# Optimization experiments

Measured on AMD Instinct MI355X. Metric: run time of the kernel, lower is better.

The kernel has to match this reference:

```python
import jax, jax.numpy as jnp
import numpy as np

HIDDEN = 128
POOL = 64
G = 4            # grid_size
NBHD = 2.0       # neighborhood_size (meters)
NUM_SCENES = 256
PEDS = 64        # pedestrians per scene (uniform seq_start_end)


def setup_inputs() -> dict:
    key = jax.random.key(0)
    k1, k2, k3 = jax.random.split(key, 3)
    hidden_states = jax.random.normal(k1, (NUM_SCENES * PEDS, HIDDEN), jnp.float32)
    positions = jax.random.uniform(k2, (NUM_SCENES * PEDS, 2), jnp.float32)
    fan_in = HIDDEN * G * G
    weight = jax.random.normal(k3, (fan_in, POOL), jnp.float32) / np.sqrt(fan_in)
    bias = jnp.zeros((POOL,), jnp.float32)
    return {
        "hidden_states": hidden_states,
        "positions": positions,
        "weight": weight,
        "bias": bias,
        "peds_per_scene": PEDS,
    }


def reference(hidden_states, positions, weight, bias, peds_per_scene):
    total, H = hidden_states.shape
    P = peds_per_scene
    B = total // P
    h = hidden_states.reshape(B, P, H)
    p = positions.reshape(B, P, 2)

    # rel[b, i, j] = pos[j] - pos[i]  (matches curr_pos - curr_pos[i:i+1])
    rel = p[:, None, :, :] - p[:, :, None, :]            # [B, P, P, 2]
    in_range = (jnp.abs(rel[..., 0]) <= NBHD) & (jnp.abs(rel[..., 1]) <= NBHD)
    not_self = ~jnp.eye(P, dtype=bool)[None]
    mask = in_range & not_self                            # [B, P, P]

    # int() truncation == floor here since (rel + NBHD) >= 0 inside the range check
    scale = G / (2.0 * NBHD)
    gx = jnp.clip(jnp.floor((rel[..., 0] + NBHD) * scale).astype(jnp.int32), 0, G - 1)
    gy = jnp.clip(jnp.floor((rel[..., 1] + NBHD) * scale).astype(jnp.int32), 0, G - 1)
    grid_idx = gy * G + gx                                # [B, P, P]

    # scatter-add of neighbor hidden states into G*G bins via masked one-hot
    onehot = jax.nn.one_hot(grid_idx, G * G, dtype=h.dtype) * mask[..., None].astype(h.dtype)
    grid = jnp.einsum('bijg,bjh->bigh', onehot, h)        # [B, P, G*G, H]

    flat = grid.reshape(B * P, G * G * H)                 # row-major: (grid_idx, hidden)
    return flat @ weight + bias                            # [total_peds, POOL]
```

## Files before the change

kernel.cpp:

```cpp
#include <hip/hip_runtime.h>
#include <cstdint>

#define PEDS   64
#define HIDDEN 128
#define POOL   64
#define GRIDG  4
#define NBHD   2.0f

typedef unsigned short u16;
typedef unsigned int   u32;
typedef __attribute__((ext_vector_type(8))) short bf16x8;
typedef __attribute__((ext_vector_type(4))) float f32x4;

__device__ __forceinline__ u16 f2bf(float f) {
    u32 u = __float_as_uint(f);
    u += 0x7fffu + ((u >> 16) & 1u);
    return (u16)(u >> 16);
}
__device__ __forceinline__ u32 pack2bf(float a, float b) {
    return (u32)f2bf(a) | ((u32)f2bf(b) << 16);
}

__global__ __launch_bounds__(256, 3) void social_r6(
    const float* __restrict__ h, const float* __restrict__ pos,
    const float* __restrict__ w, const float* __restrict__ bias,
    float* __restrict__ out)
{
    __shared__ u16 wtab[16384];
    __shared__ u16 hwT[8192];
    __shared__ u32 wmask[4];

    const int tid  = threadIdx.x;
    const int wv   = tid >> 6;
    const int lane = tid & 63;
    const int l15  = lane & 15;
    const int q    = lane >> 4;
    const int scene = blockIdx.x >> 1;
    const int ch    = blockIdx.x & 1;

    float2 pp = ((const float2*)pos)[(size_t)scene * PEDS + lane];

    const int i = wv * 16 + l15;
    const float pxi = __shfl(pp.x, i), pyi = __shfl(pp.y, i);
    const float scale = (float)GRIDG / (2.0f * NBHD);
    u32 gpk[4] = {0u, 0u, 0u, 0u};
    u32 um = 0u;
#pragma unroll
    for (int kk = 0; kk < 2; ++kk) {
#pragma unroll
        for (int e = 0; e < 8; ++e) {
            int j = kk * 32 + q * 8 + e;
            float rx = __shfl(pp.x, j) - pxi;
            float ry = __shfl(pp.y, j) - pyi;
            u32 gb = 0xffu;
            if ((i != j) && (fabsf(rx) <= NBHD) && (fabsf(ry) <= NBHD)) {
                int gx = (int)floorf((rx + NBHD) * scale); gx = min(max(gx, 0), GRIDG - 1);
                int gy = (int)floorf((ry + NBHD) * scale); gy = min(max(gy, 0), GRIDG - 1);
                gb = (u32)(gy * GRIDG + gx);
                um |= 1u << gb;
            }
            gpk[kk * 2 + (e >> 2)] |= gb << ((e & 3) * 8);
        }
    }
#pragma unroll
    for (int off = 32; off; off >>= 1) um |= __shfl_xor(um, off);
    if (lane == 0) wmask[wv] = um;

    bf16x8 af[4];
    {
        const float* hr = h + ((size_t)scene * PEDS + wv * 16 + l15) * HIDDEN + q * 8;
#pragma unroll
        for (int st4 = 0; st4 < 4; ++st4) {
            float4 f0 = *(const float4*)(hr + st4 * 32);
            float4 f1 = *(const float4*)(hr + st4 * 32 + 4);
            union { u32 u[4]; bf16x8 v; } uu;
            uu.u[0] = pack2bf(f0.x, f0.y);
            uu.u[1] = pack2bf(f0.z, f0.w);
            uu.u[2] = pack2bf(f1.x, f1.y);
            uu.u[3] = pack2bf(f1.z, f1.w);
            af[st4] = uu.v;
        }
    }
    const float bv0 = bias[ch * 32 + l15];
    const float bv1 = bias[ch * 32 + 16 + l15];

    __syncthreads();
    u32 mask = wmask[0] | wmask[1] | wmask[2] | wmask[3];
    mask = __builtin_amdgcn_readfirstlane(mask);

    f32x4 oacc0 = (f32x4){0.f, 0.f, 0.f, 0.f};
    f32x4 oacc1 = (f32x4){0.f, 0.f, 0.f, 0.f};

    const int np = __popc(mask);
    const int nb = np ? (np + 3) >> 2 : 1;
    u32 rem = mask;

    const int tl    = tid & 127;
    const int c4    = tl & 7;
    const int koct  = tl >> 3;
    const int slot0 = (tid >> 7) * 2;

    for (int b = 0; b < nb; ++b) {
        int gs[4];
#pragma unroll
        for (int t = 0; t < 4; ++t) {
            gs[t] = rem ? (__ffs(rem) - 1) : -1;
            if (rem) rem &= rem - 1u;
        }
        if (b) __syncthreads();

#pragma unroll
        for (int tt = 0; tt < 2; ++tt) {
            int t  = slot0 + tt;
            int ge = gs[t] < 0 ? 0 : gs[t];
            const float* src = w + ((size_t)(ge * HIDDEN + koct * 8)) * POOL + ch * 32 + c4 * 4;
            float4 v[8];
#pragma unroll
            for (int e = 0; e < 8; ++e) v[e] = *(const float4*)(src + (size_t)e * POOL);
            const float* vp = (const float*)v;
            int st4 = koct >> 2, ni = c4 >> 2;
            int Lb  = (koct & 3) * 16 + (c4 & 3) * 4;
            uint4* dst = (uint4*)wtab + ((t * 4 + st4) * 2 + ni) * 64 + Lb;
#pragma unroll
            for (int ii = 0; ii < 4; ++ii) {
                dst[ii] = make_uint4(
                    pack2bf(vp[0 * 4 + ii], vp[1 * 4 + ii]),
                    pack2bf(vp[2 * 4 + ii], vp[3 * 4 + ii]),
                    pack2bf(vp[4 * 4 + ii], vp[5 * 4 + ii]),
                    pack2bf(vp[6 * 4 + ii], vp[7 * 4 + ii]));
            }
        }
        __syncthreads();

        const int kkw = wv >> 1;
        const int c4w = (wv & 1) * 2 + (q >> 1);
        const int e0  = (q & 1) * 4;
#pragma unroll
        for (int t = 0; t < 4; ++t) {
            f32x4 a10 = (f32x4){0.f, 0.f, 0.f, 0.f};
            f32x4 a11 = (f32x4){0.f, 0.f, 0.f, 0.f};
#pragma unroll
            for (int st4 = 0; st4 < 4; ++st4) {
                bf16x8 b0 = *(const bf16x8*)&wtab[(((t * 4 + st4) * 2 + 0) * 64 + lane) * 8];
                bf16x8 b1 = *(const bf16x8*)&wtab[(((t * 4 + st4) * 2 + 1) * 64 + lane) * 8];
                a10 = __builtin_amdgcn_mfma_f32_16x16x32_bf16(af[st4], b0, a10, 0, 0, 0);
                a11 = __builtin_amdgcn_mfma_f32_16x16x32_bf16(af[st4], b1, a11, 0, 0, 0);
            }
            *(uint2*)&hwT[((((t * 2 + kkw) * 4 + c4w) * 2 + 0) * 16 + l15) * 8 + e0] =
                make_uint2(pack2bf(a10[0], a10[1]), pack2bf(a10[2], a10[3]));
            *(uint2*)&hwT[((((t * 2 + kkw) * 4 + c4w) * 2 + 1) * 16 + l15) * 8 + e0] =
                make_uint2(pack2bf(a11[0], a11[1]), pack2bf(a11[2], a11[3]));
        }
        __syncthreads();

#pragma unroll
        for (int t = 0; t < 4; ++t) {
            u32 gt = (u32)gs[t];
#pragma unroll
            for (int kk = 0; kk < 2; ++kk) {
                u32 wa = gpk[kk * 2], wc = gpk[kk * 2 + 1];
                union { u16 hx[8]; bf16x8 v; } mu;
#pragma unroll
                for (int bb_ = 0; bb_ < 4; ++bb_)
                    mu.hx[bb_]     = (((wa >> (bb_ * 8)) & 0xffu) == gt) ? (u16)0x3F80 : (u16)0;
#pragma unroll
                for (int bb_ = 0; bb_ < 4; ++bb_)
                    mu.hx[4 + bb_] = (((wc >> (bb_ * 8)) & 0xffu) == gt) ? (u16)0x3F80 : (u16)0;
                bf16x8 bb0 = *(const bf16x8*)&hwT[((((t * 2 + kk) * 4 + q) * 2 + 0) * 16 + l15) * 8];
                bf16x8 bb1 = *(const bf16x8*)&hwT[((((t * 2 + kk) * 4 + q) * 2 + 1) * 16 + l15) * 8];
                oacc0 = __builtin_amdgcn_mfma_f32_16x16x32_bf16(mu.v, bb0, oacc0, 0, 0, 0);
                oacc1 = __builtin_amdgcn_mfma_f32_16x16x32_bf16(mu.v, bb1, oacc1, 0, 0, 0);
            }
        }
    }

    size_t ob = ((size_t)scene * PEDS + wv * 16 + q * 4) * POOL + ch * 32 + l15;
#pragma unroll
    for (int r = 0; r < 4; ++r) {
        out[ob + (size_t)r * POOL]      = oacc0[r] + bv0;
        out[ob + (size_t)r * POOL + 16] = oacc1[r] + bv1;
    }
}

extern "C" void kernel_launch(void* const* d_in, const int* in_sizes, int n_in,
                              void* d_out, int out_size, void* d_ws, size_t ws_size,
                              hipStream_t stream) {
    const float* h    = (const float*)d_in[0];
    const float* pos  = (const float*)d_in[1];
    const float* w    = (const float*)d_in[2];
    const float* bias = (const float*)d_in[3];
    float* out = (float*)d_out;

    const int total = in_sizes[0] / HIDDEN;
    const int B     = total / PEDS;

    hipLaunchKernelGGL(social_r6, dim3(B * 2), dim3(256), 0, stream,
                       h, pos, w, bias, out);
}
```

Measured before the change: 72.71 us.

## Prefetch weights for central grid bins before computing the occupancy mask

```diff
diff --git a/kernel.cpp b/kernel.cpp
--- a/kernel.cpp
+++ b/kernel.cpp
@@ -21,7 +21,7 @@
     return (u32)f2bf(a) | ((u32)f2bf(b) << 16);
 }
 
-__global__ __launch_bounds__(256, 3) void social_r6(
+__global__ __launch_bounds__(256, 2) void social_r7(
     const float* __restrict__ h, const float* __restrict__ pos,
     const float* __restrict__ w, const float* __restrict__ bias,
     float* __restrict__ out)
@@ -38,7 +38,47 @@
     const int scene = blockIdx.x >> 1;
     const int ch    = blockIdx.x & 1;
 
+    const u32 SPECMASK = (1u << 5) | (1u << 6) | (1u << 9) | (1u << 10);
+
     float2 pp = ((const float2*)pos)[(size_t)scene * PEDS + lane];
+    const float* hr = h + ((size_t)scene * PEDS + wv * 16 + l15) * HIDDEN + q * 8;
+    float4 hf[8];
+#pragma unroll
+    for (int st4 = 0; st4 < 4; ++st4) {
+        hf[st4 * 2]     = *(const float4*)(hr + st4 * 32);
+        hf[st4 * 2 + 1] = *(const float4*)(hr + st4 * 32 + 4);
+    }
+    const float bv0 = bias[ch * 32 + l15];
+    const float bv1 = bias[ch * 32 + 16 + l15];
+
+    const int tl    = tid & 127;
+    const int c4    = tl & 7;
+    const int koct  = tl >> 3;
+    const int slot0 = (tid >> 7) * 2;
+    {
+        const int spec[4] = {5, 6, 9, 10};
+#pragma unroll
+        for (int tt = 0; tt < 2; ++tt) {
+            int t  = slot0 + tt;
+            int ge = spec[t];
+            const float* src = w + ((size_t)(ge * HIDDEN + koct * 8)) * POOL + ch * 32 + c4 * 4;
+            float4 v[8];
+#pragma unroll
+            for (int e = 0; e < 8; ++e) v[e] = *(const float4*)(src + (size_t)e * POOL);
+            const float* vp = (const float*)v;
+            int st4 = koct >> 2, ni = c4 >> 2;
+            int Lb  = (koct & 3) * 16 + (c4 & 3) * 4;
+            uint4* dst = (uint4*)wtab + ((t * 4 + st4) * 2 + ni) * 64 + Lb;
+#pragma unroll
+            for (int ii = 0; ii < 4; ++ii) {
+                dst[ii] = make_uint4(
+                    pack2bf(vp[0 * 4 + ii], vp[1 * 4 + ii]),
+                    pack2bf(vp[2 * 4 + ii], vp[3 * 4 + ii]),
+                    pack2bf(vp[4 * 4 + ii], vp[5 * 4 + ii]),
+                    pack2bf(vp[6 * 4 + ii], vp[7 * 4 + ii]));
+            }
+        }
+    }
 
     const int i = wv * 16 + l15;
     const float pxi = __shfl(pp.x, i), pyi = __shfl(pp.y, i);
@@ -67,22 +107,15 @@
     if (lane == 0) wmask[wv] = um;
 
     bf16x8 af[4];
-    {
-        const float* hr = h + ((size_t)scene * PEDS + wv * 16 + l15) * HIDDEN + q * 8;
-#pragma unroll
-        for (int st4 = 0; st4 < 4; ++st4) {
-            float4 f0 = *(const float4*)(hr + st4 * 32);
-            float4 f1 = *(const float4*)(hr + st4 * 32 + 4);
-            union { u32 u[4]; bf16x8 v; } uu;
-            uu.u[0] = pack2bf(f0.x, f0.y);
-            uu.u[1] = pack2bf(f0.z, f0.w);
-            uu.u[2] = pack2bf(f1.x, f1.y);
-            uu.u[3] = pack2bf(f1.z, f1.w);
-            af[st4] = uu.v;
-        }
-    }
-    const float bv0 = bias[ch * 32 + l15];
-    const float bv1 = bias[ch * 32 + 16 + l15];
+#pragma unroll
+    for (int st4 = 0; st4 < 4; ++st4) {
+        union { u32 u[4]; bf16x8 v; } uu;
+        uu.u[0] = pack2bf(hf[st4 * 2].x,     hf[st4 * 2].y);
+        uu.u[1] = pack2bf(hf[st4 * 2].z,     hf[st4 * 2].w);
+        uu.u[2] = pack2bf(hf[st4 * 2 + 1].x, hf[st4 * 2 + 1].y);
+        uu.u[3] = pack2bf(hf[st4 * 2 + 1].z, hf[st4 * 2 + 1].w);
+        af[st4] = uu.v;
+    }
 
     __syncthreads();
     u32 mask = wmask[0] | wmask[1] | wmask[2] | wmask[3];
@@ -91,24 +124,60 @@
     f32x4 oacc0 = (f32x4){0.f, 0.f, 0.f, 0.f};
     f32x4 oacc1 = (f32x4){0.f, 0.f, 0.f, 0.f};
 
-    const int np = __popc(mask);
-    const int nb = np ? (np + 3) >> 2 : 1;
-    u32 rem = mask;
-
-    const int tl    = tid & 127;
-    const int c4    = tl & 7;
-    const int koct  = tl >> 3;
-    const int slot0 = (tid >> 7) * 2;
-
-    for (int b = 0; b < nb; ++b) {
+    const int kkw = wv >> 1;
+    const int jqw = (wv & 1) * 2 + (q >> 1);
+    const int e0  = (q & 1) * 4;
+
+#pragma unroll
+    for (int t = 0; t < 4; ++t) {
+        f32x4 a10 = (f32x4){0.f, 0.f, 0.f, 0.f};
+        f32x4 a11 = (f32x4){0.f, 0.f, 0.f, 0.f};
+#pragma unroll
+        for (int st4 = 0; st4 < 4; ++st4) {
+            bf16x8 b0 = *(const bf16x8*)&wtab[(((t * 4 + st4) * 2 + 0) * 64 + lane) * 8];
+            bf16x8 b1 = *(const bf16x8*)&wtab[(((t * 4 + st4) * 2 + 1) * 64 + lane) * 8];
+            a10 = __builtin_amdgcn_mfma_f32_16x16x32_bf16(af[st4], b0, a10, 0, 0, 0);
+            a11 = __builtin_amdgcn_mfma_f32_16x16x32_bf16(af[st4], b1, a11, 0, 0, 0);
+        }
+        *(uint2*)&hwT[((((t * 2 + kkw) * 4 + jqw) * 2 + 0) * 16 + l15) * 8 + e0] =
+            make_uint2(pack2bf(a10[0], a10[1]), pack2bf(a10[2], a10[3]));
+        *(uint2*)&hwT[((((t * 2 + kkw) * 4 + jqw) * 2 + 1) * 16 + l15) * 8 + e0] =
+            make_uint2(pack2bf(a11[0], a11[1]), pack2bf(a11[2], a11[3]));
+    }
+    __syncthreads();
+
+    {
+        const int spec[4] = {5, 6, 9, 10};
+#pragma unroll
+        for (int t = 0; t < 4; ++t) {
+            u32 gt = (u32)spec[t];
+#pragma unroll
+            for (int kk = 0; kk < 2; ++kk) {
+                u32 wa = gpk[kk * 2], wc = gpk[kk * 2 + 1];
+                union { u16 hx[8]; bf16x8 v; } mu;
+#pragma unroll
+                for (int bb_ = 0; bb_ < 4; ++bb_)
+                    mu.hx[bb_]     = (((wa >> (bb_ * 8)) & 0xffu) == gt) ? (u16)0x3F80 : (u16)0;
+#pragma unroll
+                for (int bb_ = 0; bb_ < 4; ++bb_)
+                    mu.hx[4 + bb_] = (((wc >> (bb_ * 8)) & 0xffu) == gt) ? (u16)0x3F80 : (u16)0;
+                bf16x8 bb0 = *(const bf16x8*)&hwT[((((t * 2 + kk) * 4 + q) * 2 + 0) * 16 + l15) * 8];
+                bf16x8 bb1 = *(const bf16x8*)&hwT[((((t * 2 + kk) * 4 + q) * 2 + 1) * 16 + l15) * 8];
+                oacc0 = __builtin_amdgcn_mfma_f32_16x16x32_bf16(mu.v, bb0, oacc0, 0, 0, 0);
+                oacc1 = __builtin_amdgcn_mfma_f32_16x16x32_bf16(mu.v, bb1, oacc1, 0, 0, 0);
+            }
+        }
+    }
+
+    u32 rem = mask & ~SPECMASK;
+    while (rem) {
         int gs[4];
 #pragma unroll
         for (int t = 0; t < 4; ++t) {
             gs[t] = rem ? (__ffs(rem) - 1) : -1;
             if (rem) rem &= rem - 1u;
         }
-        if (b) __syncthreads();
-
+        __syncthreads();
 #pragma unroll
         for (int tt = 0; tt < 2; ++tt) {
             int t  = slot0 + tt;
@@ -131,10 +200,6 @@
             }
         }
         __syncthreads();
-
-        const int kkw = wv >> 1;
-        const int c4w = (wv & 1) * 2 + (q >> 1);
-        const int e0  = (q & 1) * 4;
 #pragma unroll
         for (int t = 0; t < 4; ++t) {
             f32x4 a10 = (f32x4){0.f, 0.f, 0.f, 0.f};
@@ -146,13 +211,12 @@
                 a10 = __builtin_amdgcn_mfma_f32_16x16x32_bf16(af[st4], b0, a10, 0, 0, 0);
                 a11 = __builtin_amdgcn_mfma_f32_16x16x32_bf16(af[st4], b1, a11, 0, 0, 0);
             }
-            *(uint2*)&hwT[((((t * 2 + kkw) * 4 + c4w) * 2 + 0) * 16 + l15) * 8 + e0] =
+            *(uint2*)&hwT[((((t * 2 + kkw) * 4 + jqw) * 2 + 0) * 16 + l15) * 8 + e0] =
                 make_uint2(pack2bf(a10[0], a10[1]), pack2bf(a10[2], a10[3]));
-            *(uint2*)&hwT[((((t * 2 + kkw) * 4 + c4w) * 2 + 1) * 16 + l15) * 8 + e0] =
+            *(uint2*)&hwT[((((t * 2 + kkw) * 4 + jqw) * 2 + 1) * 16 + l15) * 8 + e0] =
                 make_uint2(pack2bf(a11[0], a11[1]), pack2bf(a11[2], a11[3]));
         }
         __syncthreads();
-
 #pragma unroll
         for (int t = 0; t < 4; ++t) {
             u32 gt = (u32)gs[t];
@@ -194,6 +258,6 @@
     const int total = in_sizes[0] / HIDDEN;
     const int B     = total / PEDS;
 
-    hipLaunchKernelGGL(social_r6, dim3(B * 2), dim3(256), 0, stream,
+    hipLaunchKernelGGL(social_r7, dim3(B * 2), dim3(256), 0, stream,
                        h, pos, w, bias, out);
 }
```

Result: no change. 72.68 us (-0.0%).
